# Performance work log

Measured on AMD Instinct MI355X. Metric: run time of the kernel, lower is better.

Reference implementation:

```python
import jax, jax.numpy as jnp
import numpy as np

GROUP_SIZE = 128
SCALE_MIN = 1e-8
IN_FEATURES = 4096
OUT_FEATURES = 4096
BATCH, SEQ = 4, 2048


def quantize_literati(weight, scales):
    """w -> sign(w) * clamp(scale) per group of GROUP_SIZE along last dim.
    in_features is divisible by GROUP_SIZE, so no padding branch is needed.
    """
    O, C = weight.shape
    wg = weight.reshape(O, C // GROUP_SIZE, GROUP_SIZE)
    # torch.sign with zeros mapped to +1
    signs = jnp.where(wg >= 0, 1.0, -1.0).astype(weight.dtype)
    s = jnp.maximum(scales, SCALE_MIN)  # (O, num_groups)
    w_q = signs * s[..., None]
    return w_q.reshape(O, C)


def setup_inputs() -> dict:
    key = jax.random.key(0)
    kx, kw = jax.random.split(key)
    x = jax.random.normal(kx, (BATCH, SEQ, IN_FEATURES), dtype=jnp.float32)
    # kaiming_uniform_(a=sqrt(5)) -> U(-1/sqrt(fan_in), 1/sqrt(fan_in))
    bound = 1.0 / np.sqrt(IN_FEATURES)
    weight = jax.random.uniform(kw, (OUT_FEATURES, IN_FEATURES), dtype=jnp.float32,
                                minval=-bound, maxval=bound)
    scales = jnp.full((OUT_FEATURES, IN_FEATURES // GROUP_SIZE), 0.1, dtype=jnp.float32)
    return {"x": x, "weight": weight, "scales": scales}


def reference(x, weight, scales):
    w_q = quantize_literati(weight, scales)
    # F.linear: x @ w_q.T
    return jnp.einsum('bsc,oc->bso', x, w_q)
```

## Files before the change

kernel.cpp:

```cpp
#include <hip/hip_runtime.h>
#include <hip/hip_bf16.h>
#include <stdint.h>
#include <stddef.h>


#define M_DIM 8192
#define N_DIM 4096
#define K_DIM 4096
#define BM 256
#define BN 256
#define BK 32
#define NT (K_DIM / BK)

typedef __bf16 bf16x8 __attribute__((ext_vector_type(8)));
typedef float f32x16 __attribute__((ext_vector_type(16)));

__device__ __forceinline__ void async_copy16(const void* g, void* l) {
  __builtin_amdgcn_global_load_lds((__attribute__((address_space(1))) void*)g,
                                   (__attribute__((address_space(3))) void*)l,
                                   16, 0, 0);
}

#define X_THREADS ((size_t)M_DIM * K_DIM / 16)
#define W_THREADS ((size_t)N_DIM * K_DIM / 16)
__global__ __launch_bounds__(256) void prep_kernel(
    const float* __restrict__ x, const float* __restrict__ w,
    const float* __restrict__ scales, __bf16* __restrict__ xb,
    __bf16* __restrict__ wb) {
  const size_t t = (size_t)blockIdx.x * blockDim.x + threadIdx.x;
  if (t < X_THREADS) {
    const float4* src = (const float4*)x + t * 4;
    bf16x8* dst = (bf16x8*)xb + t * 2;
#pragma unroll
    for (int h = 0; h < 2; ++h) {
      const float4 v0 = src[h * 2 + 0];
      const float4 v1 = src[h * 2 + 1];
      bf16x8 o;
      o[0] = (__bf16)v0.x; o[1] = (__bf16)v0.y;
      o[2] = (__bf16)v0.z; o[3] = (__bf16)v0.w;
      o[4] = (__bf16)v1.x; o[5] = (__bf16)v1.y;
      o[6] = (__bf16)v1.z; o[7] = (__bf16)v1.w;
      dst[h] = o;
    }
  } else {
    const size_t u = t - X_THREADS;
    const size_t idx = u * 16;
    const int o_ = (int)(idx >> 12);
    const int grp = (int)(idx & 4095) >> 7;
    const float s = fmaxf(scales[(o_ << 5) + grp], 1e-8f);
    const float4* src = (const float4*)w + u * 4;
    bf16x8* dst = (bf16x8*)wb + u * 2;
#pragma unroll
    for (int h = 0; h < 2; ++h) {
      const float4 v0 = src[h * 2 + 0];
      const float4 v1 = src[h * 2 + 1];
      bf16x8 q;
      q[0] = (__bf16)((v0.x >= 0.f) ? s : -s);
      q[1] = (__bf16)((v0.y >= 0.f) ? s : -s);
      q[2] = (__bf16)((v0.z >= 0.f) ? s : -s);
      q[3] = (__bf16)((v0.w >= 0.f) ? s : -s);
      q[4] = (__bf16)((v1.x >= 0.f) ? s : -s);
      q[5] = (__bf16)((v1.y >= 0.f) ? s : -s);
      q[6] = (__bf16)((v1.z >= 0.f) ? s : -s);
      q[7] = (__bf16)((v1.w >= 0.f) ? s : -s);
      dst[h] = q;
    }
  }
}


#define LDS_A(b) ((char*)lds + (b) * 32768)
#define LDS_B(b) ((char*)lds + (b) * 32768 + 16384)

#define STAGE_A_TO(b) do {                        \
    char* _d = LDS_A(b);                          \
    async_copy16(aP0, _d + dO0);                  \
    async_copy16(aP1, _d + dO1);                  \
  } while (0)

#define STAGE_B_TO(b) do {                        \
    char* _d = LDS_B(b);                          \
    async_copy16(bP0, _d + dO0);                  \
    async_copy16(bP1, _d + dO1);                  \
  } while (0)

#define ADVANCE do { aP0 += BK; aP1 += BK; bP0 += BK; bP1 += BK; } while (0)

#define TILE_BODY(BUF, DO_STAGE, DO_READN, VMSTR) do {                         \
    char* _bA = LDS_A(BUF);                                                    \
    char* _bB = LDS_B(BUF);                                                    \
    char* _nA = LDS_A((BUF + 1) & 3);                                          \
    char* _nB = LDS_B((BUF + 1) & 3);                                          \
                 \
    _Pragma("unroll") for (int _i = 0; _i < 4; ++_i)                           \
      F1a[_i] = *(const bf16x8*)(_bA + aOff[_i][1]);                           \
    _Pragma("unroll") for (int _j = 0; _j < 2; ++_j)                           \
      F1b[_j] = *(const bf16x8*)(_bB + bOff[_j][1]);                           \
    if (DO_STAGE) STAGE_A_TO((BUF + 3) & 3);                                   \
    __builtin_amdgcn_s_setprio(1);                                             \
    _Pragma("unroll") for (int _i = 0; _i < 4; ++_i)                           \
      _Pragma("unroll") for (int _j = 0; _j < 2; ++_j)                         \
        acc[_i][_j] = __builtin_amdgcn_mfma_f32_32x32x16_bf16(                 \
            F0a[_i], F0b[_j], acc[_i][_j], 0, 0, 0);                           \
    __builtin_amdgcn_s_setprio(0);                                             \
                 \
    if (DO_READN) {                                                            \
      _Pragma("unroll") for (int _i = 0; _i < 4; ++_i)                         \
        F0a[_i] = *(const bf16x8*)(_nA + aOff[_i][0]);                         \
      _Pragma("unroll") for (int _j = 0; _j < 2; ++_j)                         \
        F0b[_j] = *(const bf16x8*)(_nB + bOff[_j][0]);                         \
    }                                                                          \
    if (DO_STAGE) { STAGE_B_TO((BUF + 3) & 3); ADVANCE; }                      \
    __builtin_amdgcn_s_setprio(1);                                             \
    _Pragma("unroll") for (int _i = 0; _i < 4; ++_i)                           \
      _Pragma("unroll") for (int _j = 0; _j < 2; ++_j)                         \
        acc[_i][_j] = __builtin_amdgcn_mfma_f32_32x32x16_bf16(                 \
            F1a[_i], F1b[_j], acc[_i][_j], 0, 0, 0);                           \
    __builtin_amdgcn_s_setprio(0);                                             \
    asm volatile("s_waitcnt " VMSTR ::: "memory");                             \
    __builtin_amdgcn_s_barrier();                                              \
    __builtin_amdgcn_sched_barrier(0);                \
  } while (0)

__global__ __launch_bounds__(512, 2) void literati_gemm(
    const __bf16* __restrict__ Ab, const __bf16* __restrict__ Bb,
    float* __restrict__ C) {
  __shared__ __align__(16) char lds[4 * 32768];

  const int tid = threadIdx.x;
  const int lane = tid & 63;
  const int wave = tid >> 6;
  const int bn0 = blockIdx.x * BN;
  const int bm0 = blockIdx.y * BM;
  const int wm = wave >> 2;
  const int wn = wave & 3;

  const int r_in = lane >> 2;
  const int kc_st = (lane & 3) ^ ((lane >> 3) & 3);
  const int c0 = wave * 2;
  const __bf16* aP0 = Ab + (size_t)(bm0 + c0 * 16 + r_in) * K_DIM + kc_st * 8;
  const __bf16* aP1 = Ab + (size_t)(bm0 + (c0 + 1) * 16 + r_in) * K_DIM + kc_st * 8;
  const __bf16* bP0 = Bb + (size_t)(bn0 + c0 * 16 + r_in) * K_DIM + kc_st * 8;
  const __bf16* bP1 = Bb + (size_t)(bn0 + (c0 + 1) * 16 + r_in) * K_DIM + kc_st * 8;
  const int dO0 = (c0 * 64 + lane) * 16;
  const int dO1 = ((c0 + 1) * 64 + lane) * 16;

  const int m32 = lane & 31;
  const int hl = lane >> 5;
  int aOff[4][2], bOff[2][2];
#pragma unroll
  for (int i = 0; i < 4; ++i) {
    const int row = wm * 128 + i * 32 + m32;
#pragma unroll
    for (int ks = 0; ks < 2; ++ks) {
      const int kc = 2 * ks + hl;
      aOff[i][ks] = (row * 4 + (kc ^ ((row >> 1) & 3))) * 16;
    }
  }
#pragma unroll
  for (int j = 0; j < 2; ++j) {
    const int row = wn * 64 + j * 32 + m32;
#pragma unroll
    for (int ks = 0; ks < 2; ++ks) {
      const int kc = 2 * ks + hl;
      bOff[j][ks] = (row * 4 + (kc ^ ((row >> 1) & 3))) * 16;
    }
  }

  f32x16 acc[4][2];
#pragma unroll
  for (int i = 0; i < 4; ++i)
#pragma unroll
    for (int j = 0; j < 2; ++j)
#pragma unroll
      for (int r = 0; r < 16; ++r) acc[i][j][r] = 0.f;

  bf16x8 F0a[4], F0b[2], F1a[4], F1b[2];

  STAGE_A_TO(0); STAGE_B_TO(0); ADVANCE;
  STAGE_A_TO(1); STAGE_B_TO(1); ADVANCE;
  STAGE_A_TO(2); STAGE_B_TO(2); ADVANCE;
  asm volatile("s_waitcnt vmcnt(4)" ::: "memory");
  __builtin_amdgcn_s_barrier();
  __builtin_amdgcn_sched_barrier(0);
#pragma unroll
  for (int i = 0; i < 4; ++i)
    F0a[i] = *(const bf16x8*)(LDS_A(0) + aOff[i][0]);
#pragma unroll
  for (int j = 0; j < 2; ++j)
    F0b[j] = *(const bf16x8*)(LDS_B(0) + bOff[j][0]);

  for (int tq = 0; tq < 31; ++tq) {
    TILE_BODY(0, 1, 1, "vmcnt(4)");
    TILE_BODY(1, 1, 1, "vmcnt(4)");
    TILE_BODY(2, 1, 1, "vmcnt(4)");
    TILE_BODY(3, 1, 1, "vmcnt(4)");
  }
  TILE_BODY(0, 1, 1, "vmcnt(4)");
  TILE_BODY(1, 0, 1, "vmcnt(0)");
  TILE_BODY(2, 0, 1, "vmcnt(0)");
  TILE_BODY(3, 0, 0, "vmcnt(0)");

#pragma unroll
  for (int i = 0; i < 4; ++i) {
#pragma unroll
    for (int j = 0; j < 2; ++j) {
      const int col = bn0 + wn * 64 + j * 32 + m32;
      const int rbase = bm0 + wm * 128 + i * 32 + 4 * hl;
#pragma unroll
      for (int r = 0; r < 16; ++r) {
        const int row = rbase + (r & 3) + 8 * (r >> 2);
        C[(size_t)row * N_DIM + col] = acc[i][j][r];
      }
    }
  }
}

extern "C" void kernel_launch(void* const* d_in, const int* in_sizes, int n_in,
                              void* d_out, int out_size, void* d_ws, size_t ws_size,
                              hipStream_t stream) {
  (void)in_sizes; (void)n_in; (void)out_size; (void)ws_size;
  const float* x = (const float*)d_in[0];
  const float* w = (const float*)d_in[1];
  const float* sc = (const float*)d_in[2];
  float* out = (float*)d_out;

  __bf16* xb = (__bf16*)d_ws;
  __bf16* wb = xb + (size_t)M_DIM * K_DIM;

  const size_t total_threads = X_THREADS + W_THREADS;
  prep_kernel<<<(int)(total_threads / 256), 256, 0, stream>>>(x, w, sc, xb, wb);

  dim3 grid(N_DIM / BN, M_DIM / BM);
  literati_gemm<<<grid, 512, 0, stream>>>(xb, wb, out);
}
```

Baseline: 481.5 us.

## Shrink GEMM tile to 256x128 with 4 waves, triple-buffer LDS, swizzle blocks

The GEMM block tile drops from 256x256 with 8 waves to 256x128 with 4 waves. The LDS ring shrinks from 4 stages to 3, and the cross-tile register prefetch of fragments is replaced by in-tile LDS reads. Block indices are remapped with a grouped swizzle to improve L2 reuse. The prep kernel is rewritten to coalesced float4-per-thread accesses with 4 iterations per thread. Smaller tiles double the grid and reduce per-block data reuse, and dropping the fragment prefetch may expose LDS latency.

New measurement: 526.0 us. +9.2%, slower.

```diff
diff --git a/kernel.cpp b/kernel.cpp
--- a/kernel.cpp
+++ b/kernel.cpp
@@ -8,11 +8,12 @@
 #define N_DIM 4096
 #define K_DIM 4096
 #define BM 256
-#define BN 256
+#define BN 128
 #define BK 32
 #define NT (K_DIM / BK)
 
 typedef __bf16 bf16x8 __attribute__((ext_vector_type(8)));
+typedef __bf16 bf16x4 __attribute__((ext_vector_type(4)));
 typedef float f32x16 __attribute__((ext_vector_type(16)));
 
 __device__ __forceinline__ void async_copy16(const void* g, void* l) {
@@ -21,129 +22,122 @@
                                    16, 0, 0);
 }
 
-#define X_THREADS ((size_t)M_DIM * K_DIM / 16)
-#define W_THREADS ((size_t)N_DIM * K_DIM / 16)
+#define XF4 ((size_t)M_DIM * K_DIM / 4)
+#define WF4 ((size_t)N_DIM * K_DIM / 4)
 __global__ __launch_bounds__(256) void prep_kernel(
-    const float* __restrict__ x, const float* __restrict__ w,
-    const float* __restrict__ scales, __bf16* __restrict__ xb,
-    __bf16* __restrict__ wb) {
-  const size_t t = (size_t)blockIdx.x * blockDim.x + threadIdx.x;
-  if (t < X_THREADS) {
-    const float4* src = (const float4*)x + t * 4;
-    bf16x8* dst = (bf16x8*)xb + t * 2;
-#pragma unroll
-    for (int h = 0; h < 2; ++h) {
-      const float4 v0 = src[h * 2 + 0];
-      const float4 v1 = src[h * 2 + 1];
-      bf16x8 o;
-      o[0] = (__bf16)v0.x; o[1] = (__bf16)v0.y;
-      o[2] = (__bf16)v0.z; o[3] = (__bf16)v0.w;
-      o[4] = (__bf16)v1.x; o[5] = (__bf16)v1.y;
-      o[6] = (__bf16)v1.z; o[7] = (__bf16)v1.w;
-      dst[h] = o;
+    const float4* __restrict__ x4, const float4* __restrict__ w4,
+    const float* __restrict__ scales, bf16x4* __restrict__ xb4,
+    bf16x4* __restrict__ wb4) {
+  const size_t base = (size_t)blockIdx.x * 1024 + threadIdx.x;
+  if (blockIdx.x < 8192) {
+#pragma unroll
+    for (int h = 0; h < 4; ++h) {
+      const size_t i = base + h * 256;
+      const float4 v = x4[i];
+      bf16x4 o;
+      o[0] = (__bf16)v.x; o[1] = (__bf16)v.y;
+      o[2] = (__bf16)v.z; o[3] = (__bf16)v.w;
+      xb4[i] = o;
     }
   } else {
-    const size_t u = t - X_THREADS;
-    const size_t idx = u * 16;
-    const int o_ = (int)(idx >> 12);
-    const int grp = (int)(idx & 4095) >> 7;
-    const float s = fmaxf(scales[(o_ << 5) + grp], 1e-8f);
-    const float4* src = (const float4*)w + u * 4;
-    bf16x8* dst = (bf16x8*)wb + u * 2;
-#pragma unroll
-    for (int h = 0; h < 2; ++h) {
-      const float4 v0 = src[h * 2 + 0];
-      const float4 v1 = src[h * 2 + 1];
-      bf16x8 q;
-      q[0] = (__bf16)((v0.x >= 0.f) ? s : -s);
-      q[1] = (__bf16)((v0.y >= 0.f) ? s : -s);
-      q[2] = (__bf16)((v0.z >= 0.f) ? s : -s);
-      q[3] = (__bf16)((v0.w >= 0.f) ? s : -s);
-      q[4] = (__bf16)((v1.x >= 0.f) ? s : -s);
-      q[5] = (__bf16)((v1.y >= 0.f) ? s : -s);
-      q[6] = (__bf16)((v1.z >= 0.f) ? s : -s);
-      q[7] = (__bf16)((v1.w >= 0.f) ? s : -s);
-      dst[h] = q;
-    }
-  }
-}
-
-
-#define LDS_A(b) ((char*)lds + (b) * 32768)
-#define LDS_B(b) ((char*)lds + (b) * 32768 + 16384)
-
-#define STAGE_A_TO(b) do {                        \
-    char* _d = LDS_A(b);                          \
-    async_copy16(aP0, _d + dO0);                  \
-    async_copy16(aP1, _d + dO1);                  \
+#pragma unroll
+    for (int h = 0; h < 4; ++h) {
+      const size_t j = base + h * 256 - XF4;
+      const size_t idx = j * 4;
+      const int o_ = (int)(idx >> 12);
+      const int grp = (int)(idx >> 7) & 31;
+      const float s = fmaxf(scales[(o_ << 5) + grp], 1e-8f);
+      const float4 v = w4[j];
+      bf16x4 q;
+      q[0] = (__bf16)((v.x >= 0.f) ? s : -s);
+      q[1] = (__bf16)((v.y >= 0.f) ? s : -s);
+      q[2] = (__bf16)((v.z >= 0.f) ? s : -s);
+      q[3] = (__bf16)((v.w >= 0.f) ? s : -s);
+      wb4[j] = q;
+    }
+  }
+}
+
+
+#define LDS_A(b) ((char*)lds + (b) * 24576)
+#define LDS_B(b) ((char*)lds + (b) * 24576 + 16384)
+
+#define STAGE_TO(b) do {                          \
+    char* _dA = LDS_A(b);                         \
+    char* _dB = LDS_B(b);                         \
+    async_copy16(aP0, _dA + dA0);                 \
+    async_copy16(aP1, _dA + dA1);                 \
+    async_copy16(aP2, _dA + dA2);                 \
+    async_copy16(aP3, _dA + dA3);                 \
+    async_copy16(bP0, _dB + dB0);                 \
+    async_copy16(bP1, _dB + dB1);                 \
   } while (0)
 
-#define STAGE_B_TO(b) do {                        \
-    char* _d = LDS_B(b);                          \
-    async_copy16(bP0, _d + dO0);                  \
-    async_copy16(bP1, _d + dO1);                  \
+#define ADVANCE do {                              \
+    aP0 += BK; aP1 += BK; aP2 += BK; aP3 += BK;   \
+    bP0 += BK; bP1 += BK;                         \
   } while (0)
 
-#define ADVANCE do { aP0 += BK; aP1 += BK; bP0 += BK; bP1 += BK; } while (0)
-
-#define TILE_BODY(BUF, DO_STAGE, DO_READN, VMSTR) do {                         \
+#define TILE_BODY(BUF, DO_STAGE, VMSTR) do {                                   \
     char* _bA = LDS_A(BUF);                                                    \
     char* _bB = LDS_B(BUF);                                                    \
-    char* _nA = LDS_A((BUF + 1) & 3);                                          \
-    char* _nB = LDS_B((BUF + 1) & 3);                                          \
-                 \
-    _Pragma("unroll") for (int _i = 0; _i < 4; ++_i)                           \
-      F1a[_i] = *(const bf16x8*)(_bA + aOff[_i][1]);                           \
+    bf16x8 _av[4][2], _bv[2][2];                                               \
+                     \
+    _Pragma("unroll") for (int _i = 0; _i < 4; ++_i)                           \
+      _av[_i][0] = *(const bf16x8*)(_bA + aOff[_i][0]);                        \
     _Pragma("unroll") for (int _j = 0; _j < 2; ++_j)                           \
-      F1b[_j] = *(const bf16x8*)(_bB + bOff[_j][1]);                           \
-    if (DO_STAGE) STAGE_A_TO((BUF + 3) & 3);                                   \
+      _bv[_j][0] = *(const bf16x8*)(_bB + bOff[_j][0]);                        \
+    _Pragma("unroll") for (int _i = 0; _i < 4; ++_i)                           \
+      _av[_i][1] = *(const bf16x8*)(_bA + aOff[_i][1]);                        \
+    _Pragma("unroll") for (int _j = 0; _j < 2; ++_j)                           \
+      _bv[_j][1] = *(const bf16x8*)(_bB + bOff[_j][1]);                        \
+    if (DO_STAGE) { STAGE_TO((BUF + 2) % 3); ADVANCE; }                        \
     __builtin_amdgcn_s_setprio(1);                                             \
     _Pragma("unroll") for (int _i = 0; _i < 4; ++_i)                           \
       _Pragma("unroll") for (int _j = 0; _j < 2; ++_j)                         \
         acc[_i][_j] = __builtin_amdgcn_mfma_f32_32x32x16_bf16(                 \
-            F0a[_i], F0b[_j], acc[_i][_j], 0, 0, 0);                           \
-    __builtin_amdgcn_s_setprio(0);                                             \
-                 \
-    if (DO_READN) {                                                            \
-      _Pragma("unroll") for (int _i = 0; _i < 4; ++_i)                         \
-        F0a[_i] = *(const bf16x8*)(_nA + aOff[_i][0]);                         \
-      _Pragma("unroll") for (int _j = 0; _j < 2; ++_j)                         \
-        F0b[_j] = *(const bf16x8*)(_nB + bOff[_j][0]);                         \
-    }                                                                          \
-    if (DO_STAGE) { STAGE_B_TO((BUF + 3) & 3); ADVANCE; }                      \
-    __builtin_amdgcn_s_setprio(1);                                             \
+            _av[_i][0], _bv[_j][0], acc[_i][_j], 0, 0, 0);                     \
     _Pragma("unroll") for (int _i = 0; _i < 4; ++_i)                           \
       _Pragma("unroll") for (int _j = 0; _j < 2; ++_j)                         \
         acc[_i][_j] = __builtin_amdgcn_mfma_f32_32x32x16_bf16(                 \
-            F1a[_i], F1b[_j], acc[_i][_j], 0, 0, 0);                           \
+            _av[_i][1], _bv[_j][1], acc[_i][_j], 0, 0, 0);                     \
     __builtin_amdgcn_s_setprio(0);                                             \
     asm volatile("s_waitcnt " VMSTR ::: "memory");                             \
     __builtin_amdgcn_s_barrier();                                              \
     __builtin_amdgcn_sched_barrier(0);                \
   } while (0)
 
-__global__ __launch_bounds__(512, 2) void literati_gemm(
+__global__ __launch_bounds__(256, 2) void literati_gemm(
     const __bf16* __restrict__ Ab, const __bf16* __restrict__ Bb,
     float* __restrict__ C) {
-  __shared__ __align__(16) char lds[4 * 32768];
+  __shared__ __align__(16) char lds[3 * 24576];
 
   const int tid = threadIdx.x;
   const int lane = tid & 63;
   const int wave = tid >> 6;
-  const int bn0 = blockIdx.x * BN;
-  const int bm0 = blockIdx.y * BM;
-  const int wm = wave >> 2;
-  const int wn = wave & 3;
+  const int lin = blockIdx.y * 32 + blockIdx.x;
+  const int swz = (lin & 7) * 128 + (lin >> 3);
+  const int bn0 = (swz & 31) * BN;
+  const int bm0 = (swz >> 5) * BM;
+  const int wm = wave >> 1;
+  const int wn = wave & 1;
 
   const int r_in = lane >> 2;
   const int kc_st = (lane & 3) ^ ((lane >> 3) & 3);
-  const int c0 = wave * 2;
-  const __bf16* aP0 = Ab + (size_t)(bm0 + c0 * 16 + r_in) * K_DIM + kc_st * 8;
-  const __bf16* aP1 = Ab + (size_t)(bm0 + (c0 + 1) * 16 + r_in) * K_DIM + kc_st * 8;
-  const __bf16* bP0 = Bb + (size_t)(bn0 + c0 * 16 + r_in) * K_DIM + kc_st * 8;
-  const __bf16* bP1 = Bb + (size_t)(bn0 + (c0 + 1) * 16 + r_in) * K_DIM + kc_st * 8;
-  const int dO0 = (c0 * 64 + lane) * 16;
-  const int dO1 = ((c0 + 1) * 64 + lane) * 16;
+  const int sA = wave * 4;
+  const int sB = wave * 2;
+  const __bf16* aP0 = Ab + (size_t)(bm0 + (sA + 0) * 16 + r_in) * K_DIM + kc_st * 8;
+  const __bf16* aP1 = Ab + (size_t)(bm0 + (sA + 1) * 16 + r_in) * K_DIM + kc_st * 8;
+  const __bf16* aP2 = Ab + (size_t)(bm0 + (sA + 2) * 16 + r_in) * K_DIM + kc_st * 8;
+  const __bf16* aP3 = Ab + (size_t)(bm0 + (sA + 3) * 16 + r_in) * K_DIM + kc_st * 8;
+  const __bf16* bP0 = Bb + (size_t)(bn0 + (sB + 0) * 16 + r_in) * K_DIM + kc_st * 8;
+  const __bf16* bP1 = Bb + (size_t)(bn0 + (sB + 1) * 16 + r_in) * K_DIM + kc_st * 8;
+  const int dA0 = ((sA + 0) * 64 + lane) * 16;
+  const int dA1 = ((sA + 1) * 64 + lane) * 16;
+  const int dA2 = ((sA + 2) * 64 + lane) * 16;
+  const int dA3 = ((sA + 3) * 64 + lane) * 16;
+  const int dB0 = ((sB + 0) * 64 + lane) * 16;
+  const int dB1 = ((sB + 1) * 64 + lane) * 16;
 
   const int m32 = lane & 31;
   const int hl = lane >> 5;
@@ -175,31 +169,19 @@
 #pragma unroll
       for (int r = 0; r < 16; ++r) acc[i][j][r] = 0.f;
 
-  bf16x8 F0a[4], F0b[2], F1a[4], F1b[2];
-
-  STAGE_A_TO(0); STAGE_B_TO(0); ADVANCE;
-  STAGE_A_TO(1); STAGE_B_TO(1); ADVANCE;
-  STAGE_A_TO(2); STAGE_B_TO(2); ADVANCE;
-  asm volatile("s_waitcnt vmcnt(4)" ::: "memory");
+  STAGE_TO(0); ADVANCE;
+  STAGE_TO(1); ADVANCE;
+  asm volatile("s_waitcnt vmcnt(6)" ::: "memory");
   __builtin_amdgcn_s_barrier();
   __builtin_amdgcn_sched_barrier(0);
-#pragma unroll
-  for (int i = 0; i < 4; ++i)
-    F0a[i] = *(const bf16x8*)(LDS_A(0) + aOff[i][0]);
-#pragma unroll
-  for (int j = 0; j < 2; ++j)
-    F0b[j] = *(const bf16x8*)(LDS_B(0) + bOff[j][0]);
-
-  for (int tq = 0; tq < 31; ++tq) {
-    TILE_BODY(0, 1, 1, "vmcnt(4)");
-    TILE_BODY(1, 1, 1, "vmcnt(4)");
-    TILE_BODY(2, 1, 1, "vmcnt(4)");
-    TILE_BODY(3, 1, 1, "vmcnt(4)");
-  }
-  TILE_BODY(0, 1, 1, "vmcnt(4)");
-  TILE_BODY(1, 0, 1, "vmcnt(0)");
-  TILE_BODY(2, 0, 1, "vmcnt(0)");
-  TILE_BODY(3, 0, 0, "vmcnt(0)");
+
+  for (int tq = 0; tq < 42; ++tq) {
+    TILE_BODY(0, 1, "vmcnt(6)");
+    TILE_BODY(1, 1, "vmcnt(6)");
+    TILE_BODY(2, 1, "vmcnt(6)");
+  }
+  TILE_BODY(0, 0, "vmcnt(0)");
+  TILE_BODY(1, 0, "vmcnt(0)");
 
 #pragma unroll
   for (int i = 0; i < 4; ++i) {
@@ -228,9 +210,9 @@
   __bf16* xb = (__bf16*)d_ws;
   __bf16* wb = xb + (size_t)M_DIM * K_DIM;
 
-  const size_t total_threads = X_THREADS + W_THREADS;
-  prep_kernel<<<(int)(total_threads / 256), 256, 0, stream>>>(x, w, sc, xb, wb);
+  prep_kernel<<<12288, 256, 0, stream>>>((const float4*)x, (const float4*)w,
+                                         sc, (bf16x4*)xb, (bf16x4*)wb);
 
   dim3 grid(N_DIM / BN, M_DIM / BM);
-  literati_gemm<<<grid, 512, 0, stream>>>(xb, wb, out);
-}
+  literati_gemm<<<grid, 256, 0, stream>>>(xb, wb, out);
+}
```
